# Optimization experiments

Hardware: AMD Instinct MI355X
Metric: run time of the kernel (lower is better)

## Reference

```python
import jax, jax.numpy as jnp
import numpy as np

IN_C, OUT_C, K, STRIDE, PAD = 64, 128, 3, 1, 1


def setup_inputs() -> dict:
    key = jax.random.key(0)
    kx, kw = jax.random.split(key)
    x = jax.random.normal(kx, (16, IN_C, 112, 112), dtype=jnp.float32)
    scale = np.sqrt(2.0 / (IN_C * K * K)).astype(np.float32)
    weight = jax.random.normal(kw, (OUT_C, IN_C, K, K), dtype=jnp.float32) * scale
    bias = jnp.zeros((OUT_C,), dtype=jnp.float32)
    return {"x": x, "weight": weight, "bias": bias}


def reference(x, weight, bias):
    # Direct 2D convolution (cross-correlation, like torch Conv2d), NCHW layout.
    out = jax.lax.conv_general_dilated(
        x, weight,
        window_strides=(STRIDE, STRIDE),
        padding=((PAD, PAD), (PAD, PAD)),
        dimension_numbers=("NCHW", "OIHW", "NCHW"),
    )
    return out + bias[None, :, None, None]
```

## Files before the change

kernel.cpp:

```cpp
#include <hip/hip_runtime.h>
#include <stdint.h>


#define HW     112
#define PIX    12544
#define ICN    64
#define OCN    128
#define TILEP  128
#define PTILES 98
#define NBLK   1568
#define NIMG   16

#define XT_BYTES   (NIMG * PIX * ICN * 2)
#define WT_OFF     XT_BYTES
#define WT_BYTES   (9 * OCN * ICN * 2)
#define ZG_OFF     (WT_OFF + WT_BYTES)
#define XBLK       (NIMG * (PIX / 64))
#define WBLK       72

#define XW_ZROW    160
#define XW_BYTES   (161 * 128)

typedef __attribute__((ext_vector_type(8))) __bf16 bf16x8;
typedef __attribute__((ext_vector_type(4))) float  f32x4;

__device__ __forceinline__ uint32_t rne_lo(float f) {
    uint32_t u = __builtin_bit_cast(uint32_t, f);
    return (u + 0x7fffu + ((u >> 16) & 1u)) >> 16;
}
__device__ __forceinline__ uint32_t pk2(float a, float b) {
    uint32_t ub = __builtin_bit_cast(uint32_t, b);
    ub = (ub + 0x7fffu + ((ub >> 16) & 1u)) & 0xffff0000u;
    return rne_lo(a) | ub;
}

__device__ __forceinline__ void load_lds16(const void* g, void* l) {
    __builtin_amdgcn_global_load_lds(
        (const __attribute__((address_space(1))) uint32_t*)g,
        (__attribute__((address_space(3))) uint32_t*)l, 16, 0, 0);
}

__global__ void __launch_bounds__(256)
prep(const float* __restrict__ x, const float* __restrict__ w, uint8_t* __restrict__ ws) {
    const int b = blockIdx.x;
    const int t = threadIdx.x;
    uint16_t* xt = (uint16_t*)ws;
    uint16_t* wt = (uint16_t*)(ws + WT_OFF);

    if (b < XBLK) {
        const int n  = b / (PIX / 64);
        const int p0 = (b - n * (PIX / 64)) * 64;
        const int px = t >> 2;
        const int q  = t & 3;
        const float* src = x + ((size_t)n * ICN + q * 16) * PIX + p0 + px;
        float v[16];
#pragma unroll
        for (int i = 0; i < 16; ++i) v[i] = src[(size_t)i * PIX];
        uint4 u0 = make_uint4(pk2(v[0], v[1]),  pk2(v[2], v[3]),
                              pk2(v[4], v[5]),  pk2(v[6], v[7]));
        uint4 u1 = make_uint4(pk2(v[8], v[9]),  pk2(v[10], v[11]),
                              pk2(v[12], v[13]), pk2(v[14], v[15]));
        char* dst = (char*)xt + ((size_t)(n * PIX + p0 + px)) * 128 + q * 32;
        *(uint4*)dst        = u0;
        *(uint4*)(dst + 16) = u1;
    } else {
        const int wb = b - XBLK;
#pragma unroll
        for (int k = 0; k < 4; ++k) {
            int wi = wb * 1024 + k * 256 + t;
            int r  = wi >> 13;
            int oc = (wi >> 6) & 127;
            int ic = wi & 63;
            wt[wi] = (uint16_t)rne_lo(w[oc * 576 + ic * 9 + r]);
        }
        if (wb == 0 && t < 8) ((uint4*)(ws + ZG_OFF))[t] = make_uint4(0, 0, 0, 0);
    }
}

__global__ void __launch_bounds__(256)
conv_mfma(const uint8_t* __restrict__ ws, const float* __restrict__ bias,
          float* __restrict__ out) {
    __shared__ uint16_t As[2][8192];
    __shared__ __align__(16) uint8_t Xw[2][XW_BYTES];

    const char* xt = (const char*)ws;
    const char* wt = (const char*)(ws + WT_OFF);
    const char* zg = (const char*)(ws + ZG_OFF);

    const int t = threadIdx.x;
    const int b = (blockIdx.x & 7) * (NBLK / 8) + (blockIdx.x >> 3);
    const int n_img = b / PTILES;
    const int p0 = (b - n_img * PTILES) * TILEP;

    const int lane = t & 63;
    const int wave = t >> 6;
    const int lr = lane & 15;
    const int lq = lane >> 4;
    const int oc_base = (wave & 1) * 64;
    const int px_base = (wave >> 1) * 64;

    const int rowB = t >> 3;
    const int cswz = (t & 7) ^ (rowB & 7);
    const char* xsrcX  = xt + ((size_t)n_img * PIX) * 128 + cswz * 16;
    const char* waddr0 = wt + rowB * 128 + cswz * 16;
    const char* zaddr  = zg + (t & 7) * 16;

    int hh[4], wwp[4], rbase[4];
#pragma unroll
    for (int ni = 0; ni < 4; ++ni) {
        int po = px_base + ni * 16 + lr;
        int p  = p0 + po;
        int h  = p / HW;
        hh[ni]   = h;
        wwp[ni]  = p - h * HW;
        rbase[ni] = po + 1;
    }

    auto stageW = [&](int tap, int bsel) {
#pragma unroll
        for (int r2 = 0; r2 < 4; ++r2)
            load_lds16(waddr0 + tap * 16384 + r2 * 4096,
                       (char*)As[bsel] + r2 * 4096 + wave * 1024);
    };
    auto stageX = [&](int g, int bsel) {
        const int pwb = p0 + (g - 1) * HW - 1;
#pragma unroll
        for (int r2 = 0; r2 < 5; ++r2) {
            int pw = pwb + r2 * 32 + rowB;
            const char* gp = ((unsigned)pw < PIX) ? (xsrcX + (ptrdiff_t)pw * 128) : zaddr;
            load_lds16(gp, (char*)Xw[bsel] + r2 * 4096 + wave * 1024);
        }
    };

    if (t < 16)
        *(uint4*)((char*)Xw[t >> 3] + XW_ZROW * 128 + (t & 7) * 16) = make_uint4(0, 0, 0, 0);

    f32x4 acc[4][4];
    {
        f32x4 z = {0.f, 0.f, 0.f, 0.f};
#pragma unroll
        for (int i = 0; i < 4; ++i)
#pragma unroll
            for (int j = 0; j < 4; ++j) acc[i][j] = z;
    }

    stageX(0, 0);
    stageW(0, 0);
    __syncthreads();

#pragma unroll
    for (int tap = 0; tap < 9; ++tap) {
        const int g  = tap / 3;
        const int dy = g - 1;
        const int dx = tap - g * 3 - 1;

        __builtin_amdgcn_sched_barrier(0);
        __builtin_amdgcn_s_barrier();

        if (tap < 8) stageW(tap + 1, (tap + 1) & 1);
        if (tap == 0) stageX(1, 1);
        if (tap == 3) stageX(2, 0);
        __builtin_amdgcn_sched_barrier(0);
        if (tap == 0 || tap == 1 || tap == 3 || tap == 4)
            asm volatile("s_waitcnt vmcnt(9)" ::: "memory");
        else if (tap == 8)
            asm volatile("s_waitcnt vmcnt(0)" ::: "memory");
        else
            asm volatile("s_waitcnt vmcnt(4)" ::: "memory");
        __builtin_amdgcn_sched_barrier(0);

        __builtin_amdgcn_s_barrier();

        int ro[4];
#pragma unroll
        for (int ni = 0; ni < 4; ++ni) {
            bool ok = ((unsigned)(hh[ni] + dy) < HW) & ((unsigned)(wwp[ni] + dx) < HW);
            ro[ni] = ok ? (rbase[ni] + dx) : XW_ZROW;
        }

        const char* Ab = (const char*)As[tap & 1];
        const char* Xb = (const char*)Xw[g & 1];
#pragma unroll
        for (int kh = 0; kh < 2; ++kh) {
            const int cc = kh * 4 + lq;
            bf16x8 a_frag[4], b_frag[4];
#pragma unroll
            for (int mi = 0; mi < 4; ++mi) {
                int R = oc_base + mi * 16 + lr;
                a_frag[mi] = *(const bf16x8*)(Ab + R * 128 + ((cc ^ (R & 7)) * 16));
            }
#pragma unroll
            for (int ni = 0; ni < 4; ++ni)
                b_frag[ni] = *(const bf16x8*)(Xb + ro[ni] * 128 + ((cc ^ (ro[ni] & 7)) * 16));
            __builtin_amdgcn_s_setprio(1);
#pragma unroll
            for (int mi = 0; mi < 4; ++mi)
#pragma unroll
                for (int ni = 0; ni < 4; ++ni)
                    acc[mi][ni] = __builtin_amdgcn_mfma_f32_16x16x32_bf16(
                        a_frag[mi], b_frag[ni], acc[mi][ni], 0, 0, 0);
            __builtin_amdgcn_s_setprio(0);
        }
    }

#pragma unroll
    for (int mi = 0; mi < 4; ++mi) {
#pragma unroll
        for (int rg = 0; rg < 4; ++rg) {
            const int oc = oc_base + mi * 16 + lq * 4 + rg;
            const float bb = bias[oc];
            float* orow = out + ((size_t)n_img * OCN + oc) * PIX + p0 + px_base + lr;
#pragma unroll
            for (int ni = 0; ni < 4; ++ni)
                orow[ni * 16] = acc[mi][ni][rg] + bb;
        }
    }
}

extern "C" void kernel_launch(void* const* d_in, const int* in_sizes, int n_in,
                              void* d_out, int out_size, void* d_ws, size_t ws_size,
                              hipStream_t stream) {
    const float* x    = (const float*)d_in[0];
    const float* w    = (const float*)d_in[1];
    const float* bias = (const float*)d_in[2];
    float* out = (float*)d_out;
    uint8_t* ws = (uint8_t*)d_ws;

    prep<<<XBLK + WBLK, 256, 0, stream>>>(x, w, ws);
    conv_mfma<<<NBLK, 256, 0, stream>>>(ws, bias, out);
}
```

Before: 172.1 us.

## Single-buffer the input window in LDS and rotate row-group order per block

The double-buffered 161-row input window is replaced by one 131-row window holding exactly the 128 tile pixels plus two halo rows. This cuts shared memory per block enough that launch_bounds can request 3 blocks per CU. Each block also starts its three row groups at a rotated offset (b % 3), so neighbouring blocks fetch different input rows and weight taps at the same time. The cost is that input-window loads at group boundaries are no longer prefetched and sit on the critical path, so the kernel relies on the higher occupancy to hide that latency.

```diff
diff --git a/kernel.cpp b/kernel.cpp
--- a/kernel.cpp
+++ b/kernel.cpp
@@ -18,8 +18,8 @@
 #define XBLK       (NIMG * (PIX / 64))
 #define WBLK       72
 
-#define XW_ZROW    160
-#define XW_BYTES   (161 * 128)
+#define XW_ZROW    130
+#define XW_BYTES   (131 * 128)
 
 typedef __attribute__((ext_vector_type(8))) __bf16 bf16x8;
 typedef __attribute__((ext_vector_type(4))) float  f32x4;
@@ -77,11 +77,11 @@
     }
 }
 
-__global__ void __launch_bounds__(256)
+__global__ void __launch_bounds__(256, 3)
 conv_mfma(const uint8_t* __restrict__ ws, const float* __restrict__ bias,
           float* __restrict__ out) {
     __shared__ uint16_t As[2][8192];
-    __shared__ __align__(16) uint8_t Xw[2][XW_BYTES];
+    __shared__ __align__(16) uint8_t Xw[XW_BYTES];
 
     const char* xt = (const char*)ws;
     const char* wt = (const char*)(ws + WT_OFF);
@@ -91,6 +91,7 @@
     const int b = (blockIdx.x & 7) * (NBLK / 8) + (blockIdx.x >> 3);
     const int n_img = b / PTILES;
     const int p0 = (b - n_img * PTILES) * TILEP;
+    const int grot = b % 3;
 
     const int lane = t & 63;
     const int wave = t >> 6;
@@ -116,24 +117,29 @@
         rbase[ni] = po + 1;
     }
 
-    auto stageW = [&](int tap, int bsel) {
+    auto stageW = [&](int tw, int bsel) {
 #pragma unroll
         for (int r2 = 0; r2 < 4; ++r2)
-            load_lds16(waddr0 + tap * 16384 + r2 * 4096,
+            load_lds16(waddr0 + tw * 16384 + r2 * 4096,
                        (char*)As[bsel] + r2 * 4096 + wave * 1024);
     };
-    auto stageX = [&](int g, int bsel) {
-        const int pwb = p0 + (g - 1) * HW - 1;
-#pragma unroll
-        for (int r2 = 0; r2 < 5; ++r2) {
+    auto stageX = [&](int ge) {
+        const int pwb = p0 + (ge - 1) * HW - 1;
+#pragma unroll
+        for (int r2 = 0; r2 < 4; ++r2) {
             int pw = pwb + r2 * 32 + rowB;
             const char* gp = ((unsigned)pw < PIX) ? (xsrcX + (ptrdiff_t)pw * 128) : zaddr;
-            load_lds16(gp, (char*)Xw[bsel] + r2 * 4096 + wave * 1024);
+            load_lds16(gp, (char*)Xw + r2 * 4096 + wave * 1024);
+        }
+        if (rowB < 2) {
+            int pw = pwb + 128 + rowB;
+            const char* gp = ((unsigned)pw < PIX) ? (xsrcX + (ptrdiff_t)pw * 128) : zaddr;
+            load_lds16(gp, (char*)Xw + 4 * 4096 + wave * 1024);
         }
     };
 
-    if (t < 16)
-        *(uint4*)((char*)Xw[t >> 3] + XW_ZROW * 128 + (t & 7) * 16) = make_uint4(0, 0, 0, 0);
+    if (t < 8)
+        *(uint4*)((char*)Xw + XW_ZROW * 128 + t * 16) = make_uint4(0, 0, 0, 0);
 
     f32x4 acc[4][4];
     {
@@ -144,29 +150,33 @@
             for (int j = 0; j < 4; ++j) acc[i][j] = z;
     }
 
-    stageX(0, 0);
-    stageW(0, 0);
+    {
+        const int ge0 = grot;
+        stageX(ge0);
+        stageW(ge0 * 3, 0);
+    }
     __syncthreads();
 
 #pragma unroll
-    for (int tap = 0; tap < 9; ++tap) {
-        const int g  = tap / 3;
-        const int dy = g - 1;
-        const int dx = tap - g * 3 - 1;
+    for (int j = 0; j < 9; ++j) {
+        const int gslot = j / 3;
+        const int ge    = (gslot + grot) % 3;
+        const int dy    = ge - 1;
+        const int dx    = (j - gslot * 3) - 1;
+        const bool gb   = (j == 3 || j == 6);
 
         __builtin_amdgcn_sched_barrier(0);
         __builtin_amdgcn_s_barrier();
 
-        if (tap < 8) stageW(tap + 1, (tap + 1) & 1);
-        if (tap == 0) stageX(1, 1);
-        if (tap == 3) stageX(2, 0);
+        if (gb) stageX(ge);
+        if (j < 8) {
+            const int jn = j + 1;
+            const int gn = jn / 3;
+            stageW(((gn + grot) % 3) * 3 + (jn - gn * 3), jn & 1);
+        }
         __builtin_amdgcn_sched_barrier(0);
-        if (tap == 0 || tap == 1 || tap == 3 || tap == 4)
-            asm volatile("s_waitcnt vmcnt(9)" ::: "memory");
-        else if (tap == 8)
-            asm volatile("s_waitcnt vmcnt(0)" ::: "memory");
-        else
-            asm volatile("s_waitcnt vmcnt(4)" ::: "memory");
+        if (j < 8) asm volatile("s_waitcnt vmcnt(4)" ::: "memory");
+        else       asm volatile("s_waitcnt vmcnt(0)" ::: "memory");
         __builtin_amdgcn_sched_barrier(0);
 
         __builtin_amdgcn_s_barrier();
@@ -178,8 +188,7 @@
             ro[ni] = ok ? (rbase[ni] + dx) : XW_ZROW;
         }
 
-        const char* Ab = (const char*)As[tap & 1];
-        const char* Xb = (const char*)Xw[g & 1];
+        const char* Ab = (const char*)As[j & 1];
 #pragma unroll
         for (int kh = 0; kh < 2; ++kh) {
             const int cc = kh * 4 + lq;
@@ -191,7 +200,8 @@
             }
 #pragma unroll
             for (int ni = 0; ni < 4; ++ni)
-                b_frag[ni] = *(const bf16x8*)(Xb + ro[ni] * 128 + ((cc ^ (ro[ni] & 7)) * 16));
+                b_frag[ni] = *(const bf16x8*)((const char*)Xw + ro[ni] * 128
+                                              + ((cc ^ (ro[ni] & 7)) * 16));
             __builtin_amdgcn_s_setprio(1);
 #pragma unroll
             for (int mi = 0; mi < 4; ++mi)
```

Measured after the change: 170.0 us. Within noise of the previous version (-1.3%).
